# Kernel tuning notes

Hardware: AMD Instinct MI355X
Metric: run time of the kernel (lower is better)

## Reference

```python
import jax, jax.numpy as jnp
import numpy as np


def setup_inputs() -> dict:
    key = jax.random.key(0)
    k1, k2 = jax.random.split(key)
    B, C, H, W = 16, 128, 32, 32   # C == embedding_dim
    K = 2048                        # codebook size (num_embeddings)
    x = jax.random.normal(k1, (B, C, H, W), dtype=jnp.float32)
    codebook = jax.random.normal(k2, (K, C), dtype=jnp.float32)
    return {"x": x, "codebook": codebook}


def reference(x, codebook):
    # x: [B, C, H, W] -> NHWC -> flatten to [N, C]
    B, C, H, W = x.shape
    x_nhwc = jnp.transpose(x, (0, 2, 3, 1))
    x_flat = x_nhwc.reshape(-1, C)                      # [N, C]
    # Squared L2 distances via expansion (argmin-equivalent to torch.norm
    # of the broadcast difference, without the [N, K, C] intermediate):
    x_sq = jnp.sum(x_flat * x_flat, axis=1, keepdims=True)   # [N, 1]
    w_sq = jnp.sum(codebook * codebook, axis=1)              # [K]
    d2 = x_sq - 2.0 * (x_flat @ codebook.T) + w_sq           # [N, K]
    encoding_indices = jnp.argmin(d2, axis=1)                # [N]
    encodings = jax.nn.one_hot(encoding_indices, codebook.shape[0],
                               dtype=x_flat.dtype)           # [N, K]
    quantized = encodings @ codebook                         # [N, C]
    quantized = jnp.transpose(quantized.reshape(B, H, W, C), (0, 3, 1, 2))
    return encodings, quantized
```

## Files before the change

### kernel.cpp

```cpp
#include <hip/hip_runtime.h>
#include <hip/hip_bf16.h>

#define N_TOK  16384
#define KCODES 2048
#define CDIM   128
#define BM     16
#define TPB    256
#define NCW    4
#define CPW    (KCODES / NCW)
#define TPW    (CPW / 16)
#define SEEDT  8
#define CAP    64
#define DELTA  5.0f
#define ASTR   20

typedef __attribute__((ext_vector_type(8))) short bhalf8;
typedef __attribute__((ext_vector_type(4))) float facc4;

__global__ __launch_bounds__(256) void prep_kernel(const float* __restrict__ cb,
                                                   bhalf8* __restrict__ cbt,
                                                   float* __restrict__ wsq) {
    const int T   = blockIdx.x;
    const int tid = threadIdx.x;
    const int r   = tid >> 4;
    const int g   = tid & 15;
    const float4* src = (const float4*)(cb + ((size_t)(T * 16 + r)) * CDIM + g * 8);
    float4 a0 = src[0], a1 = src[1];

    float s = a0.x*a0.x + a0.y*a0.y + a0.z*a0.z + a0.w*a0.w
            + a1.x*a1.x + a1.y*a1.y + a1.z*a1.z + a1.w*a1.w;
    s += __shfl_xor(s, 1, 64);
    s += __shfl_xor(s, 2, 64);
    s += __shfl_xor(s, 4, 64);
    s += __shfl_xor(s, 8, 64);
    if (g == 0) wsq[T * 16 + r] = s;

    union { unsigned u[4]; bhalf8 v; } fu;
    __hip_bfloat162 h0 = __float22bfloat162_rn(make_float2(a0.x, a0.y));
    __hip_bfloat162 h1 = __float22bfloat162_rn(make_float2(a0.z, a0.w));
    __hip_bfloat162 h2 = __float22bfloat162_rn(make_float2(a1.x, a1.y));
    __hip_bfloat162 h3 = __float22bfloat162_rn(make_float2(a1.z, a1.w));
    fu.u[0] = *(unsigned*)&h0; fu.u[1] = *(unsigned*)&h1;
    fu.u[2] = *(unsigned*)&h2; fu.u[3] = *(unsigned*)&h3;
    const int kf = g >> 2, q = g & 3;
    cbt[(size_t)T * 256 + kf * 64 + q * 16 + r] = fu.v;
}

__global__ __launch_bounds__(TPB, 4) void argmin_kernel(const float* __restrict__ x,
                                                        const float* __restrict__ cb,
                                                        const bhalf8* __restrict__ cbt,
                                                        const float* __restrict__ wsqg,
                                                        float* __restrict__ enc,
                                                        float* __restrict__ quant) {
    __shared__ float As[CDIM][ASTR];
    __shared__ float wsqs[KCODES];
    __shared__ float redvw[NCW][BM];
    __shared__ float rowthr[BM];
    __shared__ int   cnt[BM];
    __shared__ int   candk[BM][CAP];
    __shared__ int   rowidx[BM];

    const int tid  = threadIdx.x;
    const int lane = tid & 63;
    const int w    = tid >> 6;
    const int q    = lane >> 4;
    const int r    = lane & 15;
    const int n0   = blockIdx.x * BM;
    const int b    = n0 >> 10;
    const int hw0  = n0 & 1023;
    const float4 z4 = {0.f, 0.f, 0.f, 0.f};

    {
        int m4 = (tid & 3) << 2;
        int c0 = tid >> 2;
        #pragma unroll
        for (int i = 0; i < 2; i++) {
            int c = c0 + 64 * i;
            float4 v = *(const float4*)(x + (((size_t)(b * CDIM + c)) << 10) + hw0 + m4);
            *(float4*)(&As[c][m4]) = v;
        }
    }
    #pragma unroll
    for (int i = 0; i < KCODES / TPB; i++) wsqs[i * TPB + tid] = wsqg[i * TPB + tid];
    if (tid < BM) cnt[tid] = 0;
    __syncthreads();

    bhalf8 af[4];
    {
        int m = r;
        #pragma unroll
        for (int kf = 0; kf < 4; kf++) {
            union { unsigned u[4]; bhalf8 v; } fu;
            #pragma unroll
            for (int p = 0; p < 4; p++) {
                int k = kf * 32 + q * 8 + 2 * p;
                __hip_bfloat162 h = __float22bfloat162_rn(make_float2(As[k][m], As[k + 1][m]));
                fu.u[p] = *(unsigned*)&h;
            }
            af[kf] = fu.v;
        }
    }

    const int    cw  = w * CPW;
    const size_t tb0 = (size_t)(cw >> 4) * 256;

    {
        float rmin[4];
        #pragma unroll
        for (int t = 0; t < 4; t++) rmin[t] = 3.0e38f;

        for (int t = 0; t < SEEDT; t++) {
            bhalf8 bt[4];
            #pragma unroll
            for (int kf = 0; kf < 4; kf++) bt[kf] = cbt[tb0 + (size_t)t * 256 + kf * 64 + lane];
            facc4 acc = (facc4){0.f, 0.f, 0.f, 0.f};
            #pragma unroll
            for (int kf = 0; kf < 4; kf++)
                acc = __builtin_amdgcn_mfma_f32_16x16x32_bf16(af[kf], bt[kf], acc, 0, 0, 0);
            float wv = wsqs[cw + t * 16 + r];
            #pragma unroll
            for (int i = 0; i < 4; i++)
                rmin[i] = fminf(rmin[i], fmaf(-2.f, acc[i], wv));
        }
        #pragma unroll
        for (int t = 0; t < 4; t++) {
            float v = rmin[t];
            v = fminf(v, __shfl_xor(v, 1, 64));
            v = fminf(v, __shfl_xor(v, 2, 64));
            v = fminf(v, __shfl_xor(v, 4, 64));
            v = fminf(v, __shfl_xor(v, 8, 64));
            if (r == 0) redvw[w][q * 4 + t] = v;
        }
    }
    __syncthreads();
    if (tid < BM) {
        float mv = fminf(fminf(redvw[0][tid], redvw[1][tid]),
                         fminf(redvw[2][tid], redvw[3][tid]));
        rowthr[tid] = mv + DELTA;
    }
    __syncthreads();

    {
        float thr[4];
        #pragma unroll
        for (int t = 0; t < 4; t++) thr[t] = rowthr[q * 4 + t];

        float4* fdst = (float4*)(enc + (size_t)n0 * KCODES);

        bhalf8 bcur[4], bnxt[4];
        #pragma unroll
        for (int kf = 0; kf < 4; kf++) bcur[kf] = cbt[tb0 + kf * 64 + lane];
        #pragma unroll
        for (int kf = 0; kf < 4; kf++) bnxt[kf] = cbt[tb0 + 256 + kf * 64 + lane];

        for (int t = 0; t < TPW; t++) {
            bhalf8 bn2[4];
            if (t + 2 < TPW) {
                size_t tb = tb0 + (size_t)(t + 2) * 256;
                #pragma unroll
                for (int kf = 0; kf < 4; kf++) bn2[kf] = cbt[tb + kf * 64 + lane];
            }
            fdst[t * TPB + tid] = z4;
            facc4 acc = (facc4){0.f, 0.f, 0.f, 0.f};
            #pragma unroll
            for (int kf = 0; kf < 4; kf++)
                acc = __builtin_amdgcn_mfma_f32_16x16x32_bf16(af[kf], bcur[kf], acc, 0, 0, 0);
            float wv = wsqs[cw + t * 16 + r];
            #pragma unroll
            for (int i = 0; i < 4; i++) {
                float d = fmaf(-2.f, acc[i], wv);
                if (d <= thr[i]) {
                    int row = q * 4 + i;
                    int p = atomicAdd(&cnt[row], 1);
                    if (p < CAP) candk[row][p] = cw + t * 16 + r;
                }
            }
            #pragma unroll
            for (int kf = 0; kf < 4; kf++) { bcur[kf] = bnxt[kf]; bnxt[kf] = bn2[kf]; }
        }
    }
    __syncthreads();

    for (int m = 4 * w; m < 4 * w + 4; m++) {
        int c = cnt[m];
        float bv = 3.0e38f; int bk = 0x7fffffff;
        if (c > CAP) {
            for (int k = lane; k < KCODES; k += 64) {
                float s = 0.f;
                for (int cd = 0; cd < CDIM; cd++)
                    s = fmaf(As[cd][m], cb[(size_t)k * CDIM + cd], s);
                float d = fmaf(-2.f, s, wsqs[k]);
                if (d < bv || (d == bv && k < bk)) { bv = d; bk = k; }
            }
            #pragma unroll
            for (int off = 1; off <= 32; off <<= 1) {
                float ov = __shfl_xor(bv, off, 64);
                int   ok = __shfl_xor(bk, off, 64);
                if (ov < bv || (ov == bv && ok < bk)) { bv = ov; bk = ok; }
            }
        } else {
            for (int t = 0; t < c; t++) {
                int k = candk[m][t];
                float x0 = As[lane][m], x1 = As[lane + 64][m];
                float c0 = cb[(size_t)k * CDIM + lane];
                float c1 = cb[(size_t)k * CDIM + 64 + lane];
                float s = x0 * c0 + x1 * c1;
                #pragma unroll
                for (int off = 1; off <= 32; off <<= 1) s += __shfl_xor(s, off, 64);
                float d = fmaf(-2.f, s, wsqs[k]);
                if (d < bv || (d == bv && k < bk)) { bv = d; bk = k; }
            }
        }
        if (bk == 0x7fffffff) bk = 0;
        if (lane == 0) rowidx[m] = bk;
    }
    __syncthreads();

    if (tid < BM) enc[(size_t)(n0 + tid) * KCODES + rowidx[tid]] = 1.0f;

    #pragma unroll
    for (int i = tid; i < BM * CDIM / 4; i += TPB) {
        int c  = i >> 2;
        int hq = (i & 3) << 2;
        float4 v;
        v.x = cb[(size_t)rowidx[hq + 0] * CDIM + c];
        v.y = cb[(size_t)rowidx[hq + 1] * CDIM + c];
        v.z = cb[(size_t)rowidx[hq + 2] * CDIM + c];
        v.w = cb[(size_t)rowidx[hq + 3] * CDIM + c];
        *(float4*)(quant + (((size_t)(b * CDIM + c)) << 10) + hw0 + hq) = v;
    }
}

extern "C" void kernel_launch(void* const* d_in, const int* in_sizes, int n_in,
                              void* d_out, int out_size, void* d_ws, size_t ws_size,
                              hipStream_t stream) {
    const float* x  = (const float*)d_in[0];
    const float* cb = (const float*)d_in[1];
    float* out = (float*)d_out;

    bhalf8* cbt  = (bhalf8*)d_ws;
    float*  wsqp = (float*)((char*)d_ws + 512 * 1024);

    prep_kernel<<<KCODES / 16, 256, 0, stream>>>(cb, cbt, wsqp);
    argmin_kernel<<<N_TOK / BM, TPB, 0, stream>>>(x, cb, cbt, wsqp,
                                                  out, out + (size_t)N_TOK * KCODES);
}
```

Before: 199.1 us.

## Double row tile and share LDS-staged codebook tiles across waves

The block tile grows from 16 to 32 token rows. Each group of four codebook tiles is now loaded once into a double-buffered LDS stage with global_load_lds and shared by the waves working on both 16-row halves. Before, each wave streamed its own codebook slice from global memory into registers. This halves codebook load traffic per token, but it adds a block barrier per batch, lowers the occupancy bound to 2 blocks, and cuts the candidate cap to 32, which makes the slow full-scan fallback more likely.

```diff
diff --git a/kernel.cpp b/kernel.cpp
--- a/kernel.cpp
+++ b/kernel.cpp
@@ -4,18 +4,23 @@
 #define N_TOK  16384
 #define KCODES 2048
 #define CDIM   128
-#define BM     16
+#define BM     32
 #define TPB    256
-#define NCW    4
-#define CPW    (KCODES / NCW)
-#define TPW    (CPW / 16)
-#define SEEDT  8
-#define CAP    64
+#define NTILE  (KCODES / 16)
+#define NBATCH (NTILE / 4)
+#define SEEDS  8
+#define CAP    32
 #define DELTA  5.0f
-#define ASTR   20
+#define ASTR   36
 
 typedef __attribute__((ext_vector_type(8))) short bhalf8;
 typedef __attribute__((ext_vector_type(4))) float facc4;
+
+__device__ __forceinline__ void stage16(const void* g, void* l) {
+    __builtin_amdgcn_global_load_lds(
+        (const __attribute__((address_space(1))) void*)g,
+        (__attribute__((address_space(3))) void*)l, 16, 0, 0);
+}
 
 __global__ __launch_bounds__(256) void prep_kernel(const float* __restrict__ cb,
                                                    bhalf8* __restrict__ cbt,
@@ -46,36 +51,39 @@
     cbt[(size_t)T * 256 + kf * 64 + q * 16 + r] = fu.v;
 }
 
-__global__ __launch_bounds__(TPB, 4) void argmin_kernel(const float* __restrict__ x,
+__global__ __launch_bounds__(TPB, 2) void argmin_kernel(const float* __restrict__ x,
                                                         const float* __restrict__ cb,
                                                         const bhalf8* __restrict__ cbt,
                                                         const float* __restrict__ wsqg,
                                                         float* __restrict__ enc,
                                                         float* __restrict__ quant) {
-    __shared__ float As[CDIM][ASTR];
-    __shared__ float wsqs[KCODES];
-    __shared__ float redvw[NCW][BM];
-    __shared__ float rowthr[BM];
-    __shared__ int   cnt[BM];
-    __shared__ int   candk[BM][CAP];
-    __shared__ int   rowidx[BM];
+    __shared__ float  As[CDIM][ASTR];
+    __shared__ float  wsqs[KCODES];
+    __shared__ bhalf8 stg[2][4][256];
+    __shared__ float  redvw[4][16];
+    __shared__ float  rowthr[BM];
+    __shared__ int    cnt[BM];
+    __shared__ int    candk[BM][CAP];
+    __shared__ int    rowidx[BM];
 
     const int tid  = threadIdx.x;
     const int lane = tid & 63;
     const int w    = tid >> 6;
     const int q    = lane >> 4;
     const int r    = lane & 15;
+    const int rt   = w & 1;
+    const int par  = w >> 1;
     const int n0   = blockIdx.x * BM;
     const int b    = n0 >> 10;
     const int hw0  = n0 & 1023;
     const float4 z4 = {0.f, 0.f, 0.f, 0.f};
 
     {
-        int m4 = (tid & 3) << 2;
-        int c0 = tid >> 2;
-        #pragma unroll
-        for (int i = 0; i < 2; i++) {
-            int c = c0 + 64 * i;
+        int m4 = (tid & 7) << 2;
+        int c0 = tid >> 3;
+        #pragma unroll
+        for (int i = 0; i < 4; i++) {
+            int c = c0 + 32 * i;
             float4 v = *(const float4*)(x + (((size_t)(b * CDIM + c)) << 10) + hw0 + m4);
             *(float4*)(&As[c][m4]) = v;
         }
@@ -87,7 +95,7 @@
 
     bhalf8 af[4];
     {
-        int m = r;
+        int m = rt * 16 + r;
         #pragma unroll
         for (int kf = 0; kf < 4; kf++) {
             union { unsigned u[4]; bhalf8 v; } fu;
@@ -101,23 +109,29 @@
         }
     }
 
-    const int    cw  = w * CPW;
-    const size_t tb0 = (size_t)(cw >> 4) * 256;
+    {
+        const char* gsrc = (const char*)(cbt + (size_t)w * 256);
+        char* ldst = (char*)&stg[0][w][0];
+        #pragma unroll
+        for (int kf = 0; kf < 4; kf++)
+            stage16(gsrc + kf * 1024 + (size_t)lane * 16, ldst + kf * 1024);
+    }
 
     {
         float rmin[4];
         #pragma unroll
         for (int t = 0; t < 4; t++) rmin[t] = 3.0e38f;
 
-        for (int t = 0; t < SEEDT; t++) {
+        for (int s = 0; s < SEEDS; s++) {
+            int tile = w + 4 * s;
             bhalf8 bt[4];
             #pragma unroll
-            for (int kf = 0; kf < 4; kf++) bt[kf] = cbt[tb0 + (size_t)t * 256 + kf * 64 + lane];
+            for (int kf = 0; kf < 4; kf++) bt[kf] = cbt[(size_t)tile * 256 + kf * 64 + lane];
             facc4 acc = (facc4){0.f, 0.f, 0.f, 0.f};
             #pragma unroll
             for (int kf = 0; kf < 4; kf++)
                 acc = __builtin_amdgcn_mfma_f32_16x16x32_bf16(af[kf], bt[kf], acc, 0, 0, 0);
-            float wv = wsqs[cw + t * 16 + r];
+            float wv = wsqs[tile * 16 + r];
             #pragma unroll
             for (int i = 0; i < 4; i++)
                 rmin[i] = fminf(rmin[i], fmaf(-2.f, acc[i], wv));
@@ -134,54 +148,57 @@
     }
     __syncthreads();
     if (tid < BM) {
-        float mv = fminf(fminf(redvw[0][tid], redvw[1][tid]),
-                         fminf(redvw[2][tid], redvw[3][tid]));
-        rowthr[tid] = mv + DELTA;
+        int g = tid >> 4, idx = tid & 15;
+        rowthr[tid] = fminf(redvw[g][idx], redvw[g + 2][idx]) + DELTA;
     }
     __syncthreads();
 
     {
         float thr[4];
         #pragma unroll
-        for (int t = 0; t < 4; t++) thr[t] = rowthr[q * 4 + t];
+        for (int i = 0; i < 4; i++) thr[i] = rowthr[rt * 16 + q * 4 + i];
 
         float4* fdst = (float4*)(enc + (size_t)n0 * KCODES);
 
-        bhalf8 bcur[4], bnxt[4];
-        #pragma unroll
-        for (int kf = 0; kf < 4; kf++) bcur[kf] = cbt[tb0 + kf * 64 + lane];
-        #pragma unroll
-        for (int kf = 0; kf < 4; kf++) bnxt[kf] = cbt[tb0 + 256 + kf * 64 + lane];
-
-        for (int t = 0; t < TPW; t++) {
-            bhalf8 bn2[4];
-            if (t + 2 < TPW) {
-                size_t tb = tb0 + (size_t)(t + 2) * 256;
-                #pragma unroll
-                for (int kf = 0; kf < 4; kf++) bn2[kf] = cbt[tb + kf * 64 + lane];
-            }
-            fdst[t * TPB + tid] = z4;
-            facc4 acc = (facc4){0.f, 0.f, 0.f, 0.f};
-            #pragma unroll
-            for (int kf = 0; kf < 4; kf++)
-                acc = __builtin_amdgcn_mfma_f32_16x16x32_bf16(af[kf], bcur[kf], acc, 0, 0, 0);
-            float wv = wsqs[cw + t * 16 + r];
-            #pragma unroll
-            for (int i = 0; i < 4; i++) {
-                float d = fmaf(-2.f, acc[i], wv);
-                if (d <= thr[i]) {
-                    int row = q * 4 + i;
-                    int p = atomicAdd(&cnt[row], 1);
-                    if (p < CAP) candk[row][p] = cw + t * 16 + r;
+        for (int k = 0; k < NBATCH; k++) {
+            if (k + 1 < NBATCH) {
+                int tile = (k + 1) * 4 + w;
+                const char* gsrc = (const char*)(cbt + (size_t)tile * 256);
+                char* ldst = (char*)&stg[(k + 1) & 1][w][0];
+                #pragma unroll
+                for (int kf = 0; kf < 4; kf++)
+                    stage16(gsrc + kf * 1024 + (size_t)lane * 16, ldst + kf * 1024);
+            }
+            fdst[k * 512 + tid]       = z4;
+            fdst[k * 512 + 256 + tid] = z4;
+
+            #pragma unroll
+            for (int jj = 0; jj < 2; jj++) {
+                int j = par + jj * 2;
+                bhalf8 bt[4];
+                #pragma unroll
+                for (int kf = 0; kf < 4; kf++) bt[kf] = stg[k & 1][j][kf * 64 + lane];
+                facc4 acc = (facc4){0.f, 0.f, 0.f, 0.f};
+                #pragma unroll
+                for (int kf = 0; kf < 4; kf++)
+                    acc = __builtin_amdgcn_mfma_f32_16x16x32_bf16(af[kf], bt[kf], acc, 0, 0, 0);
+                int tile = k * 4 + j;
+                float wv = wsqs[tile * 16 + r];
+                #pragma unroll
+                for (int i = 0; i < 4; i++) {
+                    float d = fmaf(-2.f, acc[i], wv);
+                    if (d <= thr[i]) {
+                        int row = rt * 16 + q * 4 + i;
+                        int p = atomicAdd(&cnt[row], 1);
+                        if (p < CAP) candk[row][p] = tile * 16 + r;
+                    }
                 }
             }
-            #pragma unroll
-            for (int kf = 0; kf < 4; kf++) { bcur[kf] = bnxt[kf]; bnxt[kf] = bn2[kf]; }
-        }
-    }
-    __syncthreads();
-
-    for (int m = 4 * w; m < 4 * w + 4; m++) {
+            __syncthreads();
+        }
+    }
+
+    for (int m = 8 * w; m < 8 * w + 8; m++) {
         int c = cnt[m];
         float bv = 3.0e38f; int bk = 0x7fffffff;
         if (c > CAP) {
@@ -220,8 +237,8 @@
 
     #pragma unroll
     for (int i = tid; i < BM * CDIM / 4; i += TPB) {
-        int c  = i >> 2;
-        int hq = (i & 3) << 2;
+        int c  = i >> 3;
+        int hq = (i & 7) << 2;
         float4 v;
         v.x = cb[(size_t)rowidx[hq + 0] * CDIM + c];
         v.y = cb[(size_t)rowidx[hq + 1] * CDIM + c];
```

New measurement: 608.4 us. +205.6%, slower.

## Split argmin kernel into separate seed, sweep and quantize kernels

Applied to the files above, without the earlier changes.

Splits the single argmin kernel into three launches. A seed kernel computes per-row distance thresholds, a sweep kernel does the full codebook scan, one-hot write and candidate refinement, and a quant kernel gathers codebook rows into the NCHW output. Thresholds and indices pass between kernels through workspace buffers. This is meant to shorten each kernel and cut its register and sync pressure, at the cost of extra launches, loading x twice and extra global round-trips.

```diff
diff --git a/kernel.cpp b/kernel.cpp
--- a/kernel.cpp
+++ b/kernel.cpp
@@ -6,8 +6,7 @@
 #define CDIM   128
 #define BM     16
 #define TPB    256
-#define NCW    4
-#define CPW    (KCODES / NCW)
+#define CPW    (KCODES / 4)
 #define TPW    (CPW / 16)
 #define SEEDT  8
 #define CAP    64
@@ -46,15 +45,94 @@
     cbt[(size_t)T * 256 + kf * 64 + q * 16 + r] = fu.v;
 }
 
-__global__ __launch_bounds__(TPB, 4) void argmin_kernel(const float* __restrict__ x,
-                                                        const float* __restrict__ cb,
-                                                        const bhalf8* __restrict__ cbt,
-                                                        const float* __restrict__ wsqg,
-                                                        float* __restrict__ enc,
-                                                        float* __restrict__ quant) {
+__global__ __launch_bounds__(TPB, 4) void seed_kernel(const float* __restrict__ x,
+                                                      const bhalf8* __restrict__ cbt,
+                                                      const float* __restrict__ wsqg,
+                                                      float* __restrict__ rowthr_g) {
+    __shared__ float As[CDIM][ASTR];
+    __shared__ float redvw[4][BM];
+
+    const int tid  = threadIdx.x;
+    const int lane = tid & 63;
+    const int w    = tid >> 6;
+    const int q    = lane >> 4;
+    const int r    = lane & 15;
+    const int n0   = blockIdx.x * BM;
+    const int b    = n0 >> 10;
+    const int hw0  = n0 & 1023;
+
+    {
+        int m4 = (tid & 3) << 2;
+        int c0 = tid >> 2;
+        #pragma unroll
+        for (int i = 0; i < 2; i++) {
+            int c = c0 + 64 * i;
+            float4 v = *(const float4*)(x + (((size_t)(b * CDIM + c)) << 10) + hw0 + m4);
+            *(float4*)(&As[c][m4]) = v;
+        }
+    }
+    __syncthreads();
+
+    bhalf8 af[4];
+    {
+        int m = r;
+        #pragma unroll
+        for (int kf = 0; kf < 4; kf++) {
+            union { unsigned u[4]; bhalf8 v; } fu;
+            #pragma unroll
+            for (int p = 0; p < 4; p++) {
+                int k = kf * 32 + q * 8 + 2 * p;
+                __hip_bfloat162 h = __float22bfloat162_rn(make_float2(As[k][m], As[k + 1][m]));
+                fu.u[p] = *(unsigned*)&h;
+            }
+            af[kf] = fu.v;
+        }
+    }
+
+    float rmin[4];
+    #pragma unroll
+    for (int t = 0; t < 4; t++) rmin[t] = 3.0e38f;
+
+    for (int t = 0; t < SEEDT; t++) {
+        int tile = w * TPW + t;
+        bhalf8 bt[4];
+        #pragma unroll
+        for (int kf = 0; kf < 4; kf++) bt[kf] = cbt[(size_t)tile * 256 + kf * 64 + lane];
+        facc4 acc = (facc4){0.f, 0.f, 0.f, 0.f};
+        #pragma unroll
+        for (int kf = 0; kf < 4; kf++)
+            acc = __builtin_amdgcn_mfma_f32_16x16x32_bf16(af[kf], bt[kf], acc, 0, 0, 0);
+        float wv = wsqg[tile * 16 + r];
+        #pragma unroll
+        for (int i = 0; i < 4; i++)
+            rmin[i] = fminf(rmin[i], fmaf(-2.f, acc[i], wv));
+    }
+    #pragma unroll
+    for (int t = 0; t < 4; t++) {
+        float v = rmin[t];
+        v = fminf(v, __shfl_xor(v, 1, 64));
+        v = fminf(v, __shfl_xor(v, 2, 64));
+        v = fminf(v, __shfl_xor(v, 4, 64));
+        v = fminf(v, __shfl_xor(v, 8, 64));
+        if (r == 0) redvw[w][q * 4 + t] = v;
+    }
+    __syncthreads();
+    if (tid < BM) {
+        float mv = fminf(fminf(redvw[0][tid], redvw[1][tid]),
+                         fminf(redvw[2][tid], redvw[3][tid]));
+        rowthr_g[n0 + tid] = mv + DELTA;
+    }
+}
+
+__global__ __launch_bounds__(TPB, 4) void sweep_kernel(const float* __restrict__ x,
+                                                       const float* __restrict__ cb,
+                                                       const bhalf8* __restrict__ cbt,
+                                                       const float* __restrict__ wsqg,
+                                                       const float* __restrict__ rowthr_g,
+                                                       float* __restrict__ enc,
+                                                       int* __restrict__ rowidx_g) {
     __shared__ float As[CDIM][ASTR];
     __shared__ float wsqs[KCODES];
-    __shared__ float redvw[NCW][BM];
     __shared__ float rowthr[BM];
     __shared__ int   cnt[BM];
     __shared__ int   candk[BM][CAP];
@@ -82,7 +160,7 @@
     }
     #pragma unroll
     for (int i = 0; i < KCODES / TPB; i++) wsqs[i * TPB + tid] = wsqg[i * TPB + tid];
-    if (tid < BM) cnt[tid] = 0;
+    if (tid < BM) { cnt[tid] = 0; rowthr[tid] = rowthr_g[n0 + tid]; }
     __syncthreads();
 
     bhalf8 af[4];
@@ -103,42 +181,6 @@
 
     const int    cw  = w * CPW;
     const size_t tb0 = (size_t)(cw >> 4) * 256;
-
-    {
-        float rmin[4];
-        #pragma unroll
-        for (int t = 0; t < 4; t++) rmin[t] = 3.0e38f;
-
-        for (int t = 0; t < SEEDT; t++) {
-            bhalf8 bt[4];
-            #pragma unroll
-            for (int kf = 0; kf < 4; kf++) bt[kf] = cbt[tb0 + (size_t)t * 256 + kf * 64 + lane];
-            facc4 acc = (facc4){0.f, 0.f, 0.f, 0.f};
-            #pragma unroll
-            for (int kf = 0; kf < 4; kf++)
-                acc = __builtin_amdgcn_mfma_f32_16x16x32_bf16(af[kf], bt[kf], acc, 0, 0, 0);
-            float wv = wsqs[cw + t * 16 + r];
-            #pragma unroll
-            for (int i = 0; i < 4; i++)
-                rmin[i] = fminf(rmin[i], fmaf(-2.f, acc[i], wv));
-        }
-        #pragma unroll
-        for (int t = 0; t < 4; t++) {
-            float v = rmin[t];
-            v = fminf(v, __shfl_xor(v, 1, 64));
-            v = fminf(v, __shfl_xor(v, 2, 64));
-            v = fminf(v, __shfl_xor(v, 4, 64));
-            v = fminf(v, __shfl_xor(v, 8, 64));
-            if (r == 0) redvw[w][q * 4 + t] = v;
-        }
-    }
-    __syncthreads();
-    if (tid < BM) {
-        float mv = fminf(fminf(redvw[0][tid], redvw[1][tid]),
-                         fminf(redvw[2][tid], redvw[3][tid]));
-        rowthr[tid] = mv + DELTA;
-    }
-    __syncthreads();
 
     {
         float thr[4];
@@ -216,17 +258,26 @@
     }
     __syncthreads();
 
-    if (tid < BM) enc[(size_t)(n0 + tid) * KCODES + rowidx[tid]] = 1.0f;
-
-    #pragma unroll
-    for (int i = tid; i < BM * CDIM / 4; i += TPB) {
+    if (tid < BM) {
+        enc[(size_t)(n0 + tid) * KCODES + rowidx[tid]] = 1.0f;
+        rowidx_g[n0 + tid] = rowidx[tid];
+    }
+}
+
+__global__ __launch_bounds__(TPB) void quant_kernel(const float* __restrict__ cb,
+                                                    const int* __restrict__ rowidx_g,
+                                                    float* __restrict__ quant) {
+    const int n0  = blockIdx.x * BM;
+    const int b   = n0 >> 10;
+    const int hw0 = n0 & 1023;
+    for (int i = threadIdx.x; i < BM * CDIM / 4; i += TPB) {
         int c  = i >> 2;
         int hq = (i & 3) << 2;
         float4 v;
-        v.x = cb[(size_t)rowidx[hq + 0] * CDIM + c];
-        v.y = cb[(size_t)rowidx[hq + 1] * CDIM + c];
-        v.z = cb[(size_t)rowidx[hq + 2] * CDIM + c];
-        v.w = cb[(size_t)rowidx[hq + 3] * CDIM + c];
+        v.x = cb[(size_t)rowidx_g[n0 + hq + 0] * CDIM + c];
+        v.y = cb[(size_t)rowidx_g[n0 + hq + 1] * CDIM + c];
+        v.z = cb[(size_t)rowidx_g[n0 + hq + 2] * CDIM + c];
+        v.w = cb[(size_t)rowidx_g[n0 + hq + 3] * CDIM + c];
         *(float4*)(quant + (((size_t)(b * CDIM + c)) << 10) + hw0 + hq) = v;
     }
 }
@@ -238,10 +289,17 @@
     const float* cb = (const float*)d_in[1];
     float* out = (float*)d_out;
 
-    bhalf8* cbt  = (bhalf8*)d_ws;
-    float*  wsqp = (float*)((char*)d_ws + 512 * 1024);
-
-    prep_kernel<<<KCODES / 16, 256, 0, stream>>>(cb, cbt, wsqp);
-    argmin_kernel<<<N_TOK / BM, TPB, 0, stream>>>(x, cb, cbt, wsqp,
-                                                  out, out + (size_t)N_TOK * KCODES);
-}
+    bhalf8* cbt      = (bhalf8*)d_ws;
+    float*  wsqp     = (float*)((char*)d_ws + 512 * 1024);
+    float*  rowthr_g = (float*)((char*)d_ws + 520 * 1024);
+    int*    rowidx_g = (int*)  ((char*)d_ws + 584 * 1024);
+
+    float* enc   = out;
+    float* quant = out + (size_t)N_TOK * KCODES;
+
+    prep_kernel <<<KCODES / 16, 256, 0, stream>>>(cb, cbt, wsqp);
+    seed_kernel <<<N_TOK / BM, TPB, 0, stream>>>(x, cbt, wsqp, rowthr_g);
+    sweep_kernel<<<N_TOK / BM, TPB, 0, stream>>>(x, cb, cbt, wsqp, rowthr_g,
+                                                 enc, rowidx_g);
+    quant_kernel<<<N_TOK / BM, TPB, 0, stream>>>(cb, rowidx_g, quant);
+}
```

Measured after the change: 209.7 us. 1.05x slower.
